# Kernel tuning notes

Measured on AMD Instinct MI355X. Metric: run time of the kernel, lower is better.

## Reference

```python
import jax, jax.numpy as jnp
import numpy as np

N = 300000  # occupied voxels
C = 64      # channels
K = 27      # 3^3 kernel offsets


def _sparse_conv(feats, W, b, nbr):
    """Minkowski-style sparse conv: gather-GEMM-scatter per kernel offset.
    feats: [N, C], W: [K, C, C], b: [C], nbr: [K, N] int indices into feats.
    Streams over the K offsets with lax.scan to avoid a [K, N, C] intermediate.
    """
    def step(acc, wk):
        w, idx = wk  # w: [C, C], idx: [N]
        return acc + feats[idx] @ w, None
    out, _ = jax.lax.scan(step, jnp.zeros(feats.shape, feats.dtype), (W, nbr))
    return out + b


def setup_inputs() -> dict:
    key = jax.random.key(0)
    k1, k2, k3, k4, k5, k6 = jax.random.split(key, 6)
    scale = 1.0 / np.sqrt(K * C)
    return {
        "x": jax.random.normal(k1, (N, C), dtype=jnp.float32),
        "W0": jax.random.normal(k2, (K, C, C), dtype=jnp.float32) * scale,
        "b0": jax.random.normal(k3, (C,), dtype=jnp.float32) * 0.01,
        "W1": jax.random.normal(k4, (K, C, C), dtype=jnp.float32) * scale,
        "b1": jax.random.normal(k5, (C,), dtype=jnp.float32) * 0.01,
        "nbr_idx": jax.random.randint(k6, (K, N), 0, N, dtype=jnp.int32),
    }


def reference(x, W0, b0, W1, b1, nbr_idx):
    # conv0 -> relu -> conv1 -> residual add (same neighbor map, stride 1)
    out = jax.nn.relu(_sparse_conv(x, W0, b0, nbr_idx))
    out = _sparse_conv(out, W1, b1, nbr_idx)
    return out + x
```

## Files before the change

kernel.cpp:

```cpp
#include <hip/hip_runtime.h>
#include <hip/hip_bf16.h>
#include <stdint.h>

#define NV 300000
#define KOFF 27
#define BM 128

typedef __bf16 bf16x8 __attribute__((ext_vector_type(8)));
typedef float f32x4 __attribute__((ext_vector_type(4)));
typedef unsigned short u16;

__device__ __forceinline__ u16 f2bf(float f) {
  uint32_t u = __float_as_uint(f);
  uint32_t r = (u + 0x7fffu + ((u >> 16) & 1u)) >> 16;
  return (u16)r;
}

__device__ __forceinline__ void async16(const void* g, void* l) {
  __builtin_amdgcn_global_load_lds(
      (const __attribute__((address_space(1))) uint32_t*)g,
      (__attribute__((address_space(3))) uint32_t*)l, 16, 0, 0);
}

__global__ void cvt_x_kernel(const float* __restrict__ x, u16* __restrict__ xb,
                             int n) {
  int i = (blockIdx.x * 256 + threadIdx.x) * 8;
  if (i >= n) return;
  const float4 a = *(const float4*)(x + i);
  const float4 b = *(const float4*)(x + i + 4);
  uint4 o;
  o.x = (uint32_t)f2bf(a.x) | ((uint32_t)f2bf(a.y) << 16);
  o.y = (uint32_t)f2bf(a.z) | ((uint32_t)f2bf(a.w) << 16);
  o.z = (uint32_t)f2bf(b.x) | ((uint32_t)f2bf(b.y) << 16);
  o.w = (uint32_t)f2bf(b.z) | ((uint32_t)f2bf(b.w) << 16);
  *(uint4*)(xb + i) = o;
}

__global__ void cvt_w_kernel(const float* __restrict__ W0,
                             const float* __restrict__ W1,
                             u16* __restrict__ W0t, u16* __restrict__ W1t) {
  int t = blockIdx.x * 256 + threadIdx.x;
  const float* W = W0;
  u16* Wt = W0t;
  if (t >= 13824) { W = W1; Wt = W1t; t -= 13824; }
  const int p = t & 7;
  const int col = (t >> 3) & 63;
  const int k = t >> 9;
  const int c = p ^ (col & 7);
  u16 h[8];
#pragma unroll
  for (int j = 0; j < 8; j++)
    h[j] = f2bf(W[((size_t)k * 64 + c * 8 + j) * 64 + col]);
  uint4 o;
  o.x = (uint32_t)h[0] | ((uint32_t)h[1] << 16);
  o.y = (uint32_t)h[2] | ((uint32_t)h[3] << 16);
  o.z = (uint32_t)h[4] | ((uint32_t)h[5] << 16);
  o.w = (uint32_t)h[6] | ((uint32_t)h[7] << 16);
  *(uint4*)(Wt + ((size_t)k * 64 + col) * 64 + p * 8) = o;
}

template <int MODE>
__global__ __launch_bounds__(256) void conv_kernel(
    const u16* __restrict__ tab,
    const u16* __restrict__ Wt,
    const float* __restrict__ bias,
    const int* __restrict__ nbr,
    const float* __restrict__ resid, void* __restrict__ outp) {
  __shared__ __align__(16) u16 lsA[2][BM * 64];
  __shared__ __align__(16) u16 lsW[2][64 * 64];
  const int t = threadIdx.x;
  const int w = t >> 6;
  const int l = t & 63;
  const int row0 = blockIdx.x * BM;

  f32x4 acc[2][4] = {};

  float bv[4];
#pragma unroll
  for (int n = 0; n < 4; n++) bv[n] = bias[n * 16 + (l & 15)];

  int idxr[4];

  auto loadIdx = [&](int k) {
#pragma unroll
    for (int q = 0; q < 4; q++) {
      const int slot = w * 4 + q;
      const int r = slot * 8 + (l >> 3);
      const int gr = row0 + r;
      idxr[q] = (gr < NV) ? nbr[(size_t)k * NV + gr] : 0;
    }
  };

  auto issueStage = [&](int bi, int k) {
#pragma unroll
    for (int q = 0; q < 4; q++) {
      const int slot = w * 4 + q;
      const int r = slot * 8 + (l >> 3);
      const int seg = (l & 7) ^ (r & 7);
      async16(tab + (size_t)idxr[q] * 64 + seg * 8,
              (char*)(&lsA[bi][0]) + slot * 1024);
    }
    const char* wsrc = (const char*)(Wt + (size_t)k * 4096);
#pragma unroll
    for (int q = 0; q < 2; q++) {
      const int slot = w * 2 + q;
      async16(wsrc + slot * 1024 + (size_t)l * 16,
              (char*)(&lsW[bi][0]) + slot * 1024);
    }
  };

  auto compute = [&](int bi) {
    const char* A = (const char*)(&lsA[bi][0]);
    const char* B = (const char*)(&lsW[bi][0]);
    bf16x8 af[2][2], bf[4][2];
#pragma unroll
    for (int n = 0; n < 4; n++) {
      const int col = n * 16 + (l & 15);
#pragma unroll
      for (int kk = 0; kk < 2; kk++) {
        const int c = kk * 4 + (l >> 4);
        bf[n][kk] = *(const bf16x8*)(B + col * 128 + ((c ^ (col & 7)) * 16));
      }
    }
#pragma unroll
    for (int m = 0; m < 2; m++) {
      const int row = w * 32 + m * 16 + (l & 15);
#pragma unroll
      for (int kk = 0; kk < 2; kk++) {
        const int c = kk * 4 + (l >> 4);
        af[m][kk] = *(const bf16x8*)(A + row * 128 + ((c ^ (row & 7)) * 16));
      }
    }
#pragma unroll
    for (int m = 0; m < 2; m++)
#pragma unroll
      for (int n = 0; n < 4; n++)
#pragma unroll
        for (int kk = 0; kk < 2; kk++)
          acc[m][n] = __builtin_amdgcn_mfma_f32_16x16x32_bf16(
              af[m][kk], bf[n][kk], acc[m][n], 0, 0, 0);
  };

  loadIdx(0);
  issueStage(0, 0);
#pragma unroll 1
  for (int k = 0; k < KOFF; k++) {
    const int bi = k & 1;
    if (k + 1 < KOFF) loadIdx(k + 1);
    asm volatile("s_waitcnt vmcnt(0)" ::: "memory");
    __syncthreads();
    if (k + 1 < KOFF) issueStage(bi ^ 1, k + 1);
    compute(bi);
  }

#pragma unroll
  for (int m = 0; m < 2; m++) {
#pragma unroll
    for (int n = 0; n < 4; n++) {
      const int col = n * 16 + (l & 15);
#pragma unroll
      for (int j = 0; j < 4; j++) {
        const int row = row0 + w * 32 + m * 16 + (l >> 4) * 4 + j;
        if (row < NV) {
          float v = acc[m][n][j] + bv[n];
          if (MODE == 0) {
            ((u16*)outp)[(size_t)row * 64 + col] = f2bf(v < 0.f ? 0.f : v);
          } else {
            ((float*)outp)[(size_t)row * 64 + col] =
                v + resid[(size_t)row * 64 + col];
          }
        }
      }
    }
  }
}

extern "C" void kernel_launch(void* const* d_in, const int* in_sizes, int n_in,
                              void* d_out, int out_size, void* d_ws,
                              size_t ws_size, hipStream_t stream) {
  const float* x = (const float*)d_in[0];
  const float* W0 = (const float*)d_in[1];
  const float* b0 = (const float*)d_in[2];
  const float* W1 = (const float*)d_in[3];
  const float* b1 = (const float*)d_in[4];
  const int* nbr = (const int*)d_in[5];

  if (ws_size < 77242368) return;
  char* ws = (char*)d_ws;
  u16* xb = (u16*)(ws);
  u16* midb = (u16*)(ws + 38400000);
  u16* W0t = (u16*)(ws + 76800000);
  u16* W1t = (u16*)(ws + 77021184);

  cvt_w_kernel<<<108, 256, 0, stream>>>(W0, W1, W0t, W1t);
  cvt_x_kernel<<<9375, 256, 0, stream>>>(x, xb, NV * 64);

  const int nblk = (NV + BM - 1) / BM;
  conv_kernel<0><<<nblk, 256, 0, stream>>>(xb, W0t, b0, nbr, nullptr, midb);
  conv_kernel<1><<<nblk, 256, 0, stream>>>(midb, W1t, b1, nbr, x, d_out);
}
```

Baseline: 372.8 us.

## Give each wave private LDS gather buffers and drop block barriers

After: 598.3 us. 1.6x slower.

```diff
diff --git a/kernel.cpp b/kernel.cpp
--- a/kernel.cpp
+++ b/kernel.cpp
@@ -46,11 +46,10 @@
   const int p = t & 7;
   const int col = (t >> 3) & 63;
   const int k = t >> 9;
-  const int c = p ^ (col & 7);
   u16 h[8];
 #pragma unroll
   for (int j = 0; j < 8; j++)
-    h[j] = f2bf(W[((size_t)k * 64 + c * 8 + j) * 64 + col]);
+    h[j] = f2bf(W[((size_t)k * 64 + p * 8 + j) * 64 + col]);
   uint4 o;
   o.x = (uint32_t)h[0] | ((uint32_t)h[1] << 16);
   o.y = (uint32_t)h[2] | ((uint32_t)h[3] << 16);
@@ -60,75 +59,66 @@
 }
 
 template <int MODE>
-__global__ __launch_bounds__(256) void conv_kernel(
+__global__ __launch_bounds__(256, 4) void conv_kernel(
     const u16* __restrict__ tab,
     const u16* __restrict__ Wt,
     const float* __restrict__ bias,
     const int* __restrict__ nbr,
     const float* __restrict__ resid, void* __restrict__ outp) {
-  __shared__ __align__(16) u16 lsA[2][BM * 64];
-  __shared__ __align__(16) u16 lsW[2][64 * 64];
+  __shared__ __align__(16) u16 lsA[2][4][32 * 64];
   const int t = threadIdx.x;
   const int w = t >> 6;
   const int l = t & 63;
-  const int row0 = blockIdx.x * BM;
+  const int row0 = blockIdx.x * BM + w * 32;
 
   f32x4 acc[2][4] = {};
-
   float bv[4];
 #pragma unroll
   for (int n = 0; n < 4; n++) bv[n] = bias[n * 16 + (l & 15)];
 
-  int idxr[4];
-
-  auto loadIdx = [&](int k) {
+  int idxA[4], idxB[4];
+
+  auto loadIdx = [&](int k, int* dst) {
 #pragma unroll
     for (int q = 0; q < 4; q++) {
-      const int slot = w * 4 + q;
-      const int r = slot * 8 + (l >> 3);
-      const int gr = row0 + r;
-      idxr[q] = (gr < NV) ? nbr[(size_t)k * NV + gr] : 0;
-    }
-  };
-
-  auto issueStage = [&](int bi, int k) {
+      const int gr = row0 + q * 8 + (l >> 3);
+      dst[q] = (gr < NV) ? nbr[(size_t)k * NV + gr] : 0;
+    }
+  };
+
+  auto issueStage = [&](int bi, const int* idx) {
 #pragma unroll
     for (int q = 0; q < 4; q++) {
-      const int slot = w * 4 + q;
-      const int r = slot * 8 + (l >> 3);
+      const int r = q * 8 + (l >> 3);
       const int seg = (l & 7) ^ (r & 7);
-      async16(tab + (size_t)idxr[q] * 64 + seg * 8,
-              (char*)(&lsA[bi][0]) + slot * 1024);
-    }
-    const char* wsrc = (const char*)(Wt + (size_t)k * 4096);
-#pragma unroll
-    for (int q = 0; q < 2; q++) {
-      const int slot = w * 2 + q;
-      async16(wsrc + slot * 1024 + (size_t)l * 16,
-              (char*)(&lsW[bi][0]) + slot * 1024);
-    }
+      async16(tab + (size_t)idx[q] * 64 + seg * 8,
+              (char*)(&lsA[bi][w][0]) + q * 1024);
+    }
+  };
+
+  bf16x8 bf[4][2];
+  auto loadB = [&](int k) {
+    const u16* B = Wt + (size_t)k * 4096;
+#pragma unroll
+    for (int n = 0; n < 4; n++)
+#pragma unroll
+      for (int kk = 0; kk < 2; kk++) {
+        const int col = n * 16 + (l & 15);
+        const int c = kk * 4 + (l >> 4);
+        bf[n][kk] = *(const bf16x8*)(B + col * 64 + c * 8);
+      }
   };
 
   auto compute = [&](int bi) {
-    const char* A = (const char*)(&lsA[bi][0]);
-    const char* B = (const char*)(&lsW[bi][0]);
-    bf16x8 af[2][2], bf[4][2];
-#pragma unroll
-    for (int n = 0; n < 4; n++) {
-      const int col = n * 16 + (l & 15);
+    const u16* A = &lsA[bi][w][0];
+    bf16x8 af[2][2];
+#pragma unroll
+    for (int m = 0; m < 2; m++) {
+      const int row = m * 16 + (l & 15);
 #pragma unroll
       for (int kk = 0; kk < 2; kk++) {
         const int c = kk * 4 + (l >> 4);
-        bf[n][kk] = *(const bf16x8*)(B + col * 128 + ((c ^ (col & 7)) * 16));
-      }
-    }
-#pragma unroll
-    for (int m = 0; m < 2; m++) {
-      const int row = w * 32 + m * 16 + (l & 15);
-#pragma unroll
-      for (int kk = 0; kk < 2; kk++) {
-        const int c = kk * 4 + (l >> 4);
-        af[m][kk] = *(const bf16x8*)(A + row * 128 + ((c ^ (row & 7)) * 16));
+        af[m][kk] = *(const bf16x8*)(A + row * 64 + ((c ^ (row & 7)) * 8));
       }
     }
 #pragma unroll
@@ -141,16 +131,27 @@
               af[m][kk], bf[n][kk], acc[m][n], 0, 0, 0);
   };
 
-  loadIdx(0);
-  issueStage(0, 0);
+  loadIdx(0, idxA);
+  asm volatile("" ::: "memory");
+  issueStage(0, idxA);
+  asm volatile("" ::: "memory");
+  loadIdx(1, idxB);
+  asm volatile("" ::: "memory");
+
 #pragma unroll 1
   for (int k = 0; k < KOFF; k++) {
-    const int bi = k & 1;
-    if (k + 1 < KOFF) loadIdx(k + 1);
-    asm volatile("s_waitcnt vmcnt(0)" ::: "memory");
-    __syncthreads();
-    if (k + 1 < KOFF) issueStage(bi ^ 1, k + 1);
-    compute(bi);
+    asm volatile("s_waitcnt lgkmcnt(0)" ::: "memory");
+    loadB(k);
+    asm volatile("" ::: "memory");
+    issueStage((k + 1) & 1, idxB);
+    asm volatile("" ::: "memory");
+    loadIdx(k + 2 < KOFF ? k + 2 : KOFF - 1, idxA);
+    asm volatile("" ::: "memory");
+    asm volatile("s_waitcnt vmcnt(8)" ::: "memory");
+    __builtin_amdgcn_sched_barrier(0);
+    compute(k & 1);
+#pragma unroll
+    for (int q = 0; q < 4; q++) idxB[q] = idxA[q];
   }
 
 #pragma unroll
@@ -160,7 +161,7 @@
       const int col = n * 16 + (l & 15);
 #pragma unroll
       for (int j = 0; j < 4; j++) {
-        const int row = row0 + w * 32 + m * 16 + (l >> 4) * 4 + j;
+        const int row = row0 + m * 16 + (l >> 4) * 4 + j;
         if (row < NV) {
           float v = acc[m][n][j] + bv[n];
           if (MODE == 0) {
```
